# Optimization experiments

Hardware: AMD Instinct MI355X
Metric: run time of the kernel (lower is better)

## Reference

```python
import jax, jax.numpy as jnp
import numpy as np

# ---- geometry constants (from init_kwargs) ----
VOL_SHAPE = (96, 96, 96)        # (Z, Y, X)
VOL_SPACING = 1.0               # mm, isotropic
N_PROJ = 180
DET_ROWS, DET_COLS = 192, 384   # (v, u)
DET_SPACING_V, DET_SPACING_U = 1.0, 1.0
SID = 750.0                     # source-isocenter distance
SDD = 1200.0                    # source-detector distance


def _proj_matrices():
    """3x4 pinhole projection matrices for a circular cone-beam trajectory."""
    cu = (DET_COLS - 1) / 2.0
    cv = (DET_ROWS - 1) / 2.0
    Kc = np.array([[SDD / DET_SPACING_U, 0.0, cu],
                   [0.0, SDD / DET_SPACING_V, cv],
                   [0.0, 0.0, 1.0]])
    mats = []
    for th in np.linspace(0.0, 2.0 * np.pi, N_PROJ, endpoint=False):
        s = SID * np.array([np.cos(th), np.sin(th), 0.0])   # source position
        ez = -s / SID                                        # optical axis -> isocenter
        ex = np.array([-np.sin(th), np.cos(th), 0.0])        # detector u axis
        ey = np.array([0.0, 0.0, 1.0])                       # detector v axis
        R = np.stack([ex, ey, ez])                           # world -> camera
        P = Kc @ np.concatenate([R, (-R @ s)[:, None]], axis=1)
        mats.append(P)
    return np.stack(mats).astype(np.float32)                # [P, 3, 4]


def _voxel_coords():
    """Homogeneous world coordinates of all voxel centers, [4, N]."""
    zs = (np.arange(VOL_SHAPE[0]) - (VOL_SHAPE[0] - 1) / 2.0) * VOL_SPACING
    ys = (np.arange(VOL_SHAPE[1]) - (VOL_SHAPE[1] - 1) / 2.0) * VOL_SPACING
    xs = (np.arange(VOL_SHAPE[2]) - (VOL_SHAPE[2] - 1) / 2.0) * VOL_SPACING
    Z, Y, X = np.meshgrid(zs, ys, xs, indexing='ij')
    pts = np.stack([X.ravel(), Y.ravel(), Z.ravel(), np.ones(X.size)])
    return pts.astype(np.float32)


def _bilinear(img, u, v):
    """Zero-padded bilinear interpolation of img[H,W] at (v,u) pixel coords."""
    H, W = img.shape
    u0 = jnp.floor(u); v0 = jnp.floor(v)
    fu = u - u0; fv = v - v0
    u0i = u0.astype(jnp.int32); v0i = v0.astype(jnp.int32)
    def at(vi, ui):
        valid = (ui >= 0) & (ui < W) & (vi >= 0) & (vi < H)
        val = img[jnp.clip(vi, 0, H - 1), jnp.clip(ui, 0, W - 1)]
        return jnp.where(valid, val, jnp.zeros((), img.dtype))
    return (at(v0i, u0i) * (1 - fu) * (1 - fv)
            + at(v0i, u0i + 1) * fu * (1 - fv)
            + at(v0i + 1, u0i) * (1 - fu) * fv
            + at(v0i + 1, u0i + 1) * fu * fv)


def _backproject_one(sino, mats, coords):
    """sino [P,H,W], mats [P,3,4], coords [4,N] -> volume [Z,Y,X]."""
    N = coords.shape[1]
    @jax.checkpoint
    def step(acc, pm_s):
        P, s = pm_s
        uvw = P @ coords                      # [3, N]
        w = uvw[2]                            # ray depth along optical axis (>0)
        u = uvw[0] / w
        v = uvw[1] / w
        acc = acc + _bilinear(s, u, v) / (w * w)  # FDK distance weighting
        return acc, None
    acc, _ = jax.lax.scan(step, jnp.zeros((N,), sino.dtype), (mats, sino))
    return acc.reshape(VOL_SHAPE)


def setup_inputs() -> dict:
    key = jax.random.key(0)
    x = jax.random.normal(key, (2, N_PROJ, DET_ROWS, DET_COLS, 1), dtype=jnp.float32)
    proj_matrices = jnp.asarray(_proj_matrices())
    return {"x": x, "proj_matrices": proj_matrices}


def reference(x, proj_matrices):
    coords = jnp.asarray(_voxel_coords())                 # [4, N]
    sinos = jnp.squeeze(x, -1)                            # [B, P, H, W]
    vols = jax.vmap(lambda s: _backproject_one(s, proj_matrices, coords))(sinos)
    return vols[..., None]                                # [B, Z, Y, X, 1]
```

## Files before the change

kernel.cpp:

```cpp
#include <hip/hip_runtime.h>

#define NPROJ 180
#define PHALF 90
#define DH 192
#define DW 384
#define VN 96
#define ZPER 4
#define TILE_U 64
#define TILE_V 14
#define TSIZE (TILE_U * TILE_V)
#define NPAIR (2 * TSIZE)
#define PSTRIDE (DH * DW)
#define BSTRIDE (NPROJ * DH * DW)

typedef float v2f __attribute__((ext_vector_type(2)));

__global__ __launch_bounds__(256) void cone_bp(
    const float* __restrict__ sino,
    const float* __restrict__ mats,
    float* __restrict__ out)
{
    __shared__ v2f tile2[NPAIR];
    __shared__ int2 anch[PHALF];

    const int tid = threadIdx.x;
    const int x = blockIdx.x * 32 + ((tid & 7) | ((tid >> 6) << 3));
    const int y = blockIdx.y * 8 + ((tid >> 3) & 7);
    const int half = (blockIdx.z >= 24) ? 1 : 0;
    const int zc = blockIdx.z - 24 * half;
    const int pbase = half * PHALF;

    const float xw = (float)x - 47.5f;
    const float yw = (float)y - 47.5f;
    const float zw0 = (float)(zc * ZPER) - 47.5f;

    const float xwc = (float)(blockIdx.x * 32) - 32.0f;
    const float ywc = (float)(blockIdx.y * 8) - 44.0f;
    const float zwc = (float)(zc * ZPER) - 46.0f;

    const float4* __restrict__ M = (const float4*)mats;

    if (tid < PHALF) {
        int p = pbase + tid;
        float4 a0 = M[p * 3 + 0];
        float4 a1 = M[p * 3 + 1];
        float4 a2 = M[p * 3 + 2];
        float unc = fmaf(a0.x, xwc, fmaf(a0.y, ywc, a0.w));
        float vnc = fmaf(a1.x, xwc, fmaf(a1.y, ywc, fmaf(a1.z, zwc, a1.w)));
        float wc  = fmaf(a2.x, xwc, fmaf(a2.y, ywc, a2.w));
        float rwc = __builtin_amdgcn_rcpf(wc);
        anch[tid] = make_int2((int)floorf(unc * rwc) - 31,
                              (int)floorf(vnc * rwc) - 6);
    }

    int V[7];
#pragma unroll
    for (int k = 0; k < 7; ++k) {
        int li = tid + 256 * k;
        int bb = (li >= TSIZE) ? 1 : 0;
        int rem = li - bb * TSIZE;
        V[k] = bb * BSTRIDE + (rem >> 6) * DW + (rem & 63);
    }

    __syncthreads();

    int cu, cv;
    {
        int2 a = anch[0];
        cu = __builtin_amdgcn_readfirstlane(a.x);
        cv = __builtin_amdgcn_readfirstlane(a.y);
    }
    v2f g[7];
    {
        const float* __restrict__ ps = sino + pbase * PSTRIDE + cv * DW + cu;
#pragma unroll
        for (int k = 0; k < 7; ++k)
            g[k] = *(const v2f*)(ps + V[k]);
    }

    float acc0[ZPER], acc1[ZPER];
#pragma unroll
    for (int k = 0; k < ZPER; ++k) { acc0[k] = 0.0f; acc1[k] = 0.0f; }

    for (int i = 0; i < PHALF; ++i) {
        __syncthreads();
#pragma unroll
        for (int k = 0; k < 7; ++k)
            tile2[tid + 256 * k] = g[k];
        const float nfu = -(float)cu;
        const float nfv = -(float)cv;
        __syncthreads();

        if (i + 1 < PHALF) {
            int2 a = anch[i + 1];
            cu = __builtin_amdgcn_readfirstlane(a.x);
            cv = __builtin_amdgcn_readfirstlane(a.y);
            const float* __restrict__ ps =
                sino + (pbase + i + 1) * PSTRIDE + cv * DW + cu;
#pragma unroll
            for (int k = 0; k < 7; ++k)
                g[k] = *(const v2f*)(ps + V[k]);
        }

        {
            const int p = pbase + i;
            float4 r0 = M[p * 3 + 0];
            float4 r1 = M[p * 3 + 1];
            float4 r2 = M[p * 3 + 2];
            float un  = fmaf(r0.x, xw, fmaf(r0.y, yw, r0.w));
            float vn0 = fmaf(r1.x, xw, fmaf(r1.y, yw, r1.w));
            float w   = fmaf(r2.x, xw, fmaf(r2.y, yw, r2.w));
            float rw  = __builtin_amdgcn_rcpf(w);
            float iw2 = rw * rw;
            float ul  = fmaf(un, rw, nfu);
            float uf  = floorf(ul);
            float fu  = ul - uf;
            int   u0l = (int)uf;
            float vb  = fmaf(fmaf(r1.z, zw0, vn0), rw, nfv);
            float dv  = r1.z * rw;

            int   o[ZPER];
            float fv[ZPER];
#pragma unroll
            for (int k = 0; k < ZPER; ++k) {
                float v  = fmaf(dv, (float)k, vb);
                float vf = floorf(v);
                fv[k] = v - vf;
                o[k] = ((int)vf << 6) + u0l;
            }
            v2f A0[ZPER], B0[ZPER], A1[ZPER], B1[ZPER];
#pragma unroll
            for (int k = 0; k < ZPER; ++k) {
                A0[k] = tile2[o[k]];
                B0[k] = tile2[o[k] + TILE_U];
                A1[k] = tile2[o[k] + TSIZE];
                B1[k] = tile2[o[k] + TSIZE + TILE_U];
            }
#pragma unroll
            for (int k = 0; k < ZPER; ++k) {
                v2f C0 = A0[k] + (B0[k] - A0[k]) * fv[k];
                v2f C1 = A1[k] + (B1[k] - A1[k]) * fv[k];
                float h0 = fmaf(C0.y - C0.x, fu, C0.x);
                float h1 = fmaf(C1.y - C1.x, fu, C1.x);
                acc0[k] = fmaf(h0, iw2, acc0[k]);
                acc1[k] = fmaf(h1, iw2, acc1[k]);
            }
        }
    }

    const int zbase = zc * ZPER;
#pragma unroll
    for (int k = 0; k < ZPER; ++k) {
        unsafeAtomicAdd(&out[(((size_t)(zbase + k)) * VN + y) * VN + x],
                        acc0[k]);
        unsafeAtomicAdd(&out[(((size_t)(VN + zbase + k)) * VN + y) * VN + x],
                        acc1[k]);
    }
}

extern "C" void kernel_launch(void* const* d_in, const int* in_sizes, int n_in,
                              void* d_out, int out_size, void* d_ws, size_t ws_size,
                              hipStream_t stream) {
    const float* sino = (const float*)d_in[0];
    const float* mats = (const float*)d_in[1];
    float* out = (float*)d_out;

    hipMemsetAsync(out, 0, (size_t)out_size * sizeof(float), stream);

    dim3 grid(VN / 32, VN / 8, 48), block(256);
    hipLaunchKernelGGL(cone_bp, grid, block, 0, stream, sino, mats, out);
}
```

Baseline: 323.6 us.

## Interleave batches in LDS tile and double-buffer to drop one barrier per projection

The shared tile now stores the two batch volumes interleaved per pixel (65x14 entries of float2) instead of storing horizontal u-pairs per batch. This cuts the global loads per projection from 7 to 4 per thread, though each load is now a scalar float per batch rather than a float2. The loop alternates between two LDS buffers so only one __syncthreads per projection is needed, and the arithmetic becomes packed v2f ops across the two batches. Launch bounds also add an occupancy hint of 6. The trade-offs are more scalar global loads and a larger LDS footprint.

```diff
diff --git a/kernel.cpp b/kernel.cpp
--- a/kernel.cpp
+++ b/kernel.cpp
@@ -6,21 +6,21 @@
 #define DW 384
 #define VN 96
 #define ZPER 4
-#define TILE_U 64
-#define TILE_V 14
-#define TSIZE (TILE_U * TILE_V)
-#define NPAIR (2 * TSIZE)
+#define TCOLS 65
+#define TROWS 14
+#define TENT (TCOLS * TROWS)
+#define TPAD 1024
 #define PSTRIDE (DH * DW)
 #define BSTRIDE (NPROJ * DH * DW)
 
 typedef float v2f __attribute__((ext_vector_type(2)));
 
-__global__ __launch_bounds__(256) void cone_bp(
+__global__ __launch_bounds__(256, 6) void cone_bp(
     const float* __restrict__ sino,
     const float* __restrict__ mats,
     float* __restrict__ out)
 {
-    __shared__ v2f tile2[NPAIR];
+    __shared__ v2f tile[2][TPAD];
     __shared__ int2 anch[PHALF];
 
     const int tid = threadIdx.x;
@@ -53,13 +53,13 @@
                               (int)floorf(vnc * rwc) - 6);
     }
 
-    int V[7];
+    int VgB[4];
 #pragma unroll
-    for (int k = 0; k < 7; ++k) {
+    for (int k = 0; k < 4; ++k) {
         int li = tid + 256 * k;
-        int bb = (li >= TSIZE) ? 1 : 0;
-        int rem = li - bb * TSIZE;
-        V[k] = bb * BSTRIDE + (rem >> 6) * DW + (rem & 63);
+        int row = li / TCOLS;
+        int col = li - row * TCOLS;
+        VgB[k] = (row * DW + col) * 4;
     }
 
     __syncthreads();
@@ -70,91 +70,98 @@
         cu = __builtin_amdgcn_readfirstlane(a.x);
         cv = __builtin_amdgcn_readfirstlane(a.y);
     }
-    v2f g[7];
+    v2f g[4];
     {
-        const float* __restrict__ ps = sino + pbase * PSTRIDE + cv * DW + cu;
+        const char* p0 = (const char*)(sino + pbase * PSTRIDE + cv * DW + cu);
+        const char* p1 = p0 + (size_t)BSTRIDE * 4;
 #pragma unroll
-        for (int k = 0; k < 7; ++k)
-            g[k] = *(const v2f*)(ps + V[k]);
+        for (int k = 0; k < 4; ++k) {
+            g[k].x = *(const float*)(p0 + VgB[k]);
+            g[k].y = *(const float*)(p1 + VgB[k]);
+        }
     }
 
-    float acc0[ZPER], acc1[ZPER];
+    v2f acc[ZPER];
 #pragma unroll
-    for (int k = 0; k < ZPER; ++k) { acc0[k] = 0.0f; acc1[k] = 0.0f; }
+    for (int k = 0; k < ZPER; ++k) acc[k] = (v2f)(0.0f);
 
-    for (int i = 0; i < PHALF; ++i) {
-        __syncthreads();
+    auto body = [&](int i, v2f* __restrict__ buf) {
 #pragma unroll
-        for (int k = 0; k < 7; ++k)
-            tile2[tid + 256 * k] = g[k];
+        for (int k = 0; k < 4; ++k)
+            buf[tid + 256 * k] = g[k];
         const float nfu = -(float)cu;
         const float nfv = -(float)cv;
-        __syncthreads();
 
         if (i + 1 < PHALF) {
             int2 a = anch[i + 1];
             cu = __builtin_amdgcn_readfirstlane(a.x);
             cv = __builtin_amdgcn_readfirstlane(a.y);
-            const float* __restrict__ ps =
-                sino + (pbase + i + 1) * PSTRIDE + cv * DW + cu;
+            const char* p0 = (const char*)(sino
+                + (pbase + i + 1) * PSTRIDE + cv * DW + cu);
+            const char* p1 = p0 + (size_t)BSTRIDE * 4;
 #pragma unroll
-            for (int k = 0; k < 7; ++k)
-                g[k] = *(const v2f*)(ps + V[k]);
+            for (int k = 0; k < 4; ++k) {
+                g[k].x = *(const float*)(p0 + VgB[k]);
+                g[k].y = *(const float*)(p1 + VgB[k]);
+            }
         }
 
-        {
-            const int p = pbase + i;
-            float4 r0 = M[p * 3 + 0];
-            float4 r1 = M[p * 3 + 1];
-            float4 r2 = M[p * 3 + 2];
-            float un  = fmaf(r0.x, xw, fmaf(r0.y, yw, r0.w));
-            float vn0 = fmaf(r1.x, xw, fmaf(r1.y, yw, r1.w));
-            float w   = fmaf(r2.x, xw, fmaf(r2.y, yw, r2.w));
-            float rw  = __builtin_amdgcn_rcpf(w);
-            float iw2 = rw * rw;
-            float ul  = fmaf(un, rw, nfu);
-            float uf  = floorf(ul);
-            float fu  = ul - uf;
-            int   u0l = (int)uf;
-            float vb  = fmaf(fmaf(r1.z, zw0, vn0), rw, nfv);
-            float dv  = r1.z * rw;
+        __syncthreads();
 
-            int   o[ZPER];
-            float fv[ZPER];
+        const int p = pbase + i;
+        float4 r0 = M[p * 3 + 0];
+        float4 r1 = M[p * 3 + 1];
+        float4 r2 = M[p * 3 + 2];
+        float un  = fmaf(r0.x, xw, fmaf(r0.y, yw, r0.w));
+        float vn0 = fmaf(r1.x, xw, fmaf(r1.y, yw, r1.w));
+        float w   = fmaf(r2.x, xw, fmaf(r2.y, yw, r2.w));
+        float rw  = __builtin_amdgcn_rcpf(w);
+        float iw2 = rw * rw;
+        float ul  = fmaf(un, rw, nfu);
+        float uf  = floorf(ul);
+        float fu  = ul - uf;
+        int   u0l = (int)uf;
+        float vb  = fmaf(fmaf(r1.z, zw0, vn0), rw, nfv);
+        float dv  = r1.z * rw;
+
+        int   o[ZPER];
+        float fv[ZPER];
 #pragma unroll
-            for (int k = 0; k < ZPER; ++k) {
-                float v  = fmaf(dv, (float)k, vb);
-                float vf = floorf(v);
-                fv[k] = v - vf;
-                o[k] = ((int)vf << 6) + u0l;
-            }
-            v2f A0[ZPER], B0[ZPER], A1[ZPER], B1[ZPER];
+        for (int k = 0; k < ZPER; ++k) {
+            float v  = fmaf(dv, (float)k, vb);
+            float vf = floorf(v);
+            fv[k] = v - vf;
+            o[k] = (int)vf * TCOLS + u0l;
+        }
+        v2f E00[ZPER], E01[ZPER], E10[ZPER], E11[ZPER];
 #pragma unroll
-            for (int k = 0; k < ZPER; ++k) {
-                A0[k] = tile2[o[k]];
-                B0[k] = tile2[o[k] + TILE_U];
-                A1[k] = tile2[o[k] + TSIZE];
-                B1[k] = tile2[o[k] + TSIZE + TILE_U];
-            }
+        for (int k = 0; k < ZPER; ++k) {
+            E00[k] = buf[o[k]];
+            E01[k] = buf[o[k] + 1];
+            E10[k] = buf[o[k] + TCOLS];
+            E11[k] = buf[o[k] + TCOLS + 1];
+        }
 #pragma unroll
-            for (int k = 0; k < ZPER; ++k) {
-                v2f C0 = A0[k] + (B0[k] - A0[k]) * fv[k];
-                v2f C1 = A1[k] + (B1[k] - A1[k]) * fv[k];
-                float h0 = fmaf(C0.y - C0.x, fu, C0.x);
-                float h1 = fmaf(C1.y - C1.x, fu, C1.x);
-                acc0[k] = fmaf(h0, iw2, acc0[k]);
-                acc1[k] = fmaf(h1, iw2, acc1[k]);
-            }
+        for (int k = 0; k < ZPER; ++k) {
+            v2f F0 = E00[k] + (E10[k] - E00[k]) * fv[k];
+            v2f F1 = E01[k] + (E11[k] - E01[k]) * fv[k];
+            v2f H  = F0 + (F1 - F0) * fu;
+            acc[k] += H * iw2;
         }
+    };
+
+    for (int i = 0; i < PHALF; i += 2) {
+        body(i,     tile[0]);
+        body(i + 1, tile[1]);
     }
 
     const int zbase = zc * ZPER;
 #pragma unroll
     for (int k = 0; k < ZPER; ++k) {
         unsafeAtomicAdd(&out[(((size_t)(zbase + k)) * VN + y) * VN + x],
-                        acc0[k]);
+                        acc[k].x);
         unsafeAtomicAdd(&out[(((size_t)(VN + zbase + k)) * VN + y) * VN + x],
-                        acc1[k]);
+                        acc[k].y);
     }
 }
 
```

After: 290.0 us. 1.12x faster.
